# Optimization experiments

Hardware: AMD Instinct MI355X
Metric: run time of the kernel (lower is better)

The kernel has to match this reference:

```python
import jax, jax.numpy as jnp
import numpy as np

NC = 6            # CPAB tessellation cells (tess_size=6, zero_boundary=True)
DIM = NC - 1      # theta dimension = 5
SIG_LEN = 2048
CHANNELS = 3
BATCH = 256
FC_IN = 64 * 168  # flattened net_part1 output for signal_len=2048
NUM_SCALING = 0   # N in transform_data_ss
EPS_BN = 1e-5


def _cpab_basis():
    """QR null-space basis of the CPAB continuity + zero-boundary constraints.
    Params ordered [a_1,b_1,...,a_NC,b_NC]; v(x)=a_c x + b_c on cell c."""
    nc = NC
    L = np.zeros((nc + 1, 2 * nc))
    for k in range(1, nc):  # continuity at internal knots x_k = k/nc
        xk = k / nc
        L[k - 1, 2 * (k - 1)] = xk
        L[k - 1, 2 * (k - 1) + 1] = 1.0
        L[k - 1, 2 * k] = -xk
        L[k - 1, 2 * k + 1] = -1.0
    L[nc - 1, 1] = 1.0        # v(0) = 0  -> b_1 = 0
    L[nc, 2 * (nc - 1)] = 1.0  # v(1) = 0 -> a_nc + b_nc = 0
    L[nc, 2 * nc - 1] = 1.0
    Q, _ = np.linalg.qr(L.T, mode='complete')
    return np.ascontiguousarray(Q[:, nc + 1:]).astype(np.float32)  # (12, 5)


def _conv1d(x, w, b):
    y = jax.lax.conv_general_dilated(x, w, (1,), 'VALID',
                                     dimension_numbers=('NCH', 'OIH', 'NCH'))
    return y + b[None, :, None]


def _maxpool1d(x, k, s):
    return jax.lax.reduce_window(x, -jnp.inf, jax.lax.max, (1, 1, k), (1, 1, s), 'VALID')


def _bn(x, g, b, m, v):  # eval-mode BatchNorm1d
    return (x - m[None, :, None]) * (g / jnp.sqrt(v + EPS_BN))[None, :, None] + b[None, :, None]


def _integrate(x, A):
    """Exact CPAB 1D flow integration over t=1 with cell-crossing handling.
    x: (B, n) points in [0,1]; A: (B, NC, 2) per-cell (a, b). Monotone
    trajectories cross at most NC-1 boundaries -> fixed NC+1 iterations."""
    a_all, b_all = A[:, :, 0], A[:, :, 1]
    t = jnp.ones_like(x)
    for _ in range(NC + 1):
        c = jnp.clip(jnp.floor(x * NC).astype(jnp.int32), 0, NC - 1)
        a = jnp.take_along_axis(a_all, c, axis=1)
        b = jnp.take_along_axis(b_all, c, axis=1)
        v = a * x + b
        xb = jnp.where(v >= 0, (c + 1).astype(x.dtype) / NC, c.astype(x.dtype) / NC)
        big_a = jnp.abs(a) > 1e-8
        a_s = jnp.where(big_a, a, 1.0)
        z = x + b / a_s        # shifted coord: x(t) = z*exp(a t) - b/a
        zb = xb + b / a_s
        ratio = zb / jnp.where(jnp.abs(z) > 1e-12, z, 1e-12)
        t_exp = jnp.log(jnp.maximum(ratio, 1e-12)) / a_s
        v_s = jnp.where(jnp.abs(v) > 1e-12, v, 1.0)
        t_lin = (xb - x) / v_s
        thit = jnp.where(big_a, t_exp, t_lin)
        valid = (jnp.abs(v) > 1e-12) & (thit > 0) & (jnp.where(big_a, ratio, 1.0) > 0)
        thit = jnp.where(valid, thit, jnp.inf)
        tau = jnp.minimum(t, thit)
        x_new = jnp.where(big_a, z * jnp.exp(a * tau) - (z - x), x + b * tau)
        hit = thit <= t
        nudge = jnp.where(v >= 0, 1e-6, -1e-6)  # push into next cell
        x = jnp.clip(jnp.where(hit, xb + nudge, x_new), 0.0, 1.0)
        t = jnp.maximum(t - tau, 0.0)
    return x


def _interp1d(data, pos):
    """data: (B, L, C); pos: (B, n) in [0,1] -> (B, n, C) linear interpolation."""
    Lw = data.shape[1]
    p = jnp.clip(pos, 0.0, 1.0) * (Lw - 1)
    x0 = jnp.clip(jnp.floor(p).astype(jnp.int32), 0, Lw - 2)
    w = (p - x0.astype(p.dtype))[:, :, None]
    d0 = jnp.take_along_axis(data, x0[:, :, None], axis=1)
    d1 = jnp.take_along_axis(data, (x0 + 1)[:, :, None], axis=1)
    return d0 * (1.0 - w) + d1 * w


def _transform_data_ss(data, theta, basis, outsize, N):
    """CPAB scaling-and-squaring warp of data (B, L, C) by theta (B, DIM)."""
    Bsz = theta.shape[0]
    A = (theta @ basis.T).reshape(Bsz, NC, 2) / (2.0 ** N)
    grid = jnp.linspace(0.0, 1.0, outsize, dtype=data.dtype)
    grid_t = _integrate(jnp.broadcast_to(grid, (Bsz, outsize)), A)
    for _ in range(N):  # squaring: compose the warp with itself
        grid_t = _interp1d(grid_t[:, :, None], grid_t)[:, :, 0]
    return _interp1d(data, grid_t)


def reference(x, conv1_w, conv1_b, bn1_g, bn1_b, bn1_m, bn1_v,
              conv2_w, conv2_b, bn2_g, bn2_b, bn2_m, bn2_v,
              conv3_w, conv3_b, bn3_g, bn3_b, bn3_m, bn3_v,
              fc1_w, fc1_b, fc2_w, fc2_b, fc3_w, fc3_b, fc4_w, fc4_b, basis):
    # localization net (n_recurrence = 1, back_version = True)
    h = jax.nn.relu(_maxpool1d(_bn(_conv1d(x, conv1_w, conv1_b), bn1_g, bn1_b, bn1_m, bn1_v), 3, 2))
    h = jax.nn.relu(_maxpool1d(_bn(_conv1d(h, conv2_w, conv2_b), bn2_g, bn2_b, bn2_m, bn2_v), 3, 3))
    h = jax.nn.relu(_maxpool1d(_bn(_conv1d(h, conv3_w, conv3_b), bn3_g, bn3_b, bn3_m, bn3_v), 3, 2))
    xs = h.reshape(h.shape[0], -1)  # (B, 64*168)
    xs = jax.nn.relu(xs @ fc1_w.T + fc1_b)
    xs = jax.nn.relu(xs @ fc2_w.T + fc2_b)
    xs = jax.nn.relu(xs @ fc3_w.T + fc3_b)
    theta = jnp.tanh(xs @ fc4_w.T + fc4_b)  # (B, 5)
    data = jnp.transpose(x, (0, 2, 1))       # (B, L, C)
    warped = _transform_data_ss(data, theta, basis, SIG_LEN, NUM_SCALING)
    return jnp.transpose(warped, (0, 2, 1))  # (B, C, L)


def setup_inputs() -> dict:
    key = jax.random.key(0)
    ks = jax.random.split(key, 16)
    def nrm(k, shape, scale):
        return (jax.random.normal(k, shape) * scale).astype(jnp.float32)
    inp = {}
    inp['x'] = jax.random.normal(ks[0], (BATCH, CHANNELS, SIG_LEN), dtype=jnp.float32)
    inp['conv1_w'] = nrm(ks[1], (128, CHANNELS, 3), (CHANNELS * 3) ** -0.5)
    inp['conv1_b'] = nrm(ks[2], (128,), 0.01)
    inp['bn1_g'] = jnp.ones((128,), jnp.float32)
    inp['bn1_b'] = jnp.zeros((128,), jnp.float32)
    inp['bn1_m'] = nrm(ks[3], (128,), 0.1)
    inp['bn1_v'] = jnp.ones((128,), jnp.float32)
    inp['conv2_w'] = nrm(ks[4], (64, 128, 5), (128 * 5) ** -0.5)
    inp['conv2_b'] = nrm(ks[5], (64,), 0.01)
    inp['bn2_g'] = jnp.ones((64,), jnp.float32)
    inp['bn2_b'] = jnp.zeros((64,), jnp.float32)
    inp['bn2_m'] = nrm(ks[6], (64,), 0.1)
    inp['bn2_v'] = jnp.ones((64,), jnp.float32)
    inp['conv3_w'] = nrm(ks[7], (64, 64, 3), (64 * 3) ** -0.5)
    inp['conv3_b'] = nrm(ks[8], (64,), 0.01)
    inp['bn3_g'] = jnp.ones((64,), jnp.float32)
    inp['bn3_b'] = jnp.zeros((64,), jnp.float32)
    inp['bn3_m'] = nrm(ks[9], (64,), 0.1)
    inp['bn3_v'] = jnp.ones((64,), jnp.float32)
    inp['fc1_w'] = nrm(ks[10], (48, FC_IN), FC_IN ** -0.5)
    inp['fc1_b'] = jnp.zeros((48,), jnp.float32)
    inp['fc2_w'] = nrm(ks[11], (32, 48), 48 ** -0.5)
    inp['fc2_b'] = jnp.zeros((32,), jnp.float32)
    inp['fc3_w'] = nrm(ks[12], (16, 32), 32 ** -0.5)
    inp['fc3_b'] = jnp.zeros((16,), jnp.float32)
    # near-identity warp head (original zero-inits weight, identity bias)
    inp['fc4_w'] = nrm(ks[13], (DIM, 16), 0.01)
    inp['fc4_b'] = nrm(ks[14], (DIM,), 0.01)
    inp['basis'] = jnp.asarray(_cpab_basis())
    return inp
```

## Files before the change

kernel.cpp:

```cpp
#include <hip/hip_runtime.h>
#include <math.h>

#define BATCH   256
#define SIGLEN  2048
#define L1OUT   1022
#define L2OUT   339
#define L3OUT   168
#define FCIN    10752

#define TP2   21
#define NROW  68
#define H1S   136

#define TU3   28

#define KC1   12
#define KCL   (FCIN/KC1)

typedef float f32x4  __attribute__((ext_vector_type(4)));
typedef float f32x16 __attribute__((ext_vector_type(16)));
typedef short s16x8  __attribute__((ext_vector_type(8)));

__device__ __forceinline__ unsigned short f2bf(float f) {
    unsigned int u = __float_as_uint(f);
    return (unsigned short)((u + 0x7fffu + ((u >> 16) & 1u)) >> 16);
}
__device__ __forceinline__ float bf2f(unsigned short h) {
    return __uint_as_float(((unsigned int)h) << 16);
}

__launch_bounds__(256)
__global__ void prep_kernel(
    const float* __restrict__ conv1_b,
    const float* __restrict__ g1, const float* __restrict__ b1,
    const float* __restrict__ m1, const float* __restrict__ v1,
    const float* __restrict__ conv2_w, const float* __restrict__ conv2_b,
    const float* __restrict__ g2, const float* __restrict__ b2,
    const float* __restrict__ m2, const float* __restrict__ v2,
    const float* __restrict__ conv3_w, const float* __restrict__ conv3_b,
    const float* __restrict__ g3, const float* __restrict__ b3,
    const float* __restrict__ m3, const float* __restrict__ v3,
    const float* __restrict__ fc1_w,
    unsigned short* __restrict__ w2hi, unsigned short* __restrict__ w2lo,
    unsigned short* __restrict__ w3hi, unsigned short* __restrict__ w3lo,
    float* __restrict__ wp1,
    float* __restrict__ so1, float* __restrict__ so2, float* __restrict__ so3)
{
    int tid = blockIdx.x * 256 + threadIdx.x;
    int stride = gridDim.x * 256;
    for (int i = tid; i < 64*128*5; i += stride) {
        int co = i / 640; int rr = i - co*640; int ci = rr / 5; int k = rr - ci*5;
        float w = conv2_w[i];
        unsigned short hi = f2bf(w);
        unsigned short lo = f2bf(w - bf2f(hi));
        int seg = k*8 + (ci >> 4);
        int dst = ((seg*2 + (co >> 5))*32 + (co & 31))*16 + (ci & 15);
        w2hi[dst] = hi;
        w2lo[dst] = lo;
    }
    for (int i = tid; i < 64*64*3; i += stride) {
        int co = i / 192; int r = i - co*192; int ci = r / 3; int k = r - ci*3;
        float w = conv3_w[i];
        unsigned short hi = f2bf(w);
        unsigned short lo = f2bf(w - bf2f(hi));
        int dst = ((k*2 + (ci >> 5))*64 + co)*32 + (ci & 31);
        w3hi[dst] = hi;
        w3lo[dst] = lo;
    }
    for (int i = tid; i < 48*FCIN; i += stride) {
        int o = i / FCIN; int r = i - o*FCIN;
        int u = r >> 6, co = r & 63;
        wp1[i] = fc1_w[o*FCIN + co*L3OUT + u];
    }
    if (tid < 128) {
        float s = g1[tid] / sqrtf(v1[tid] + 1e-5f);
        so1[tid]       = s;
        so1[128 + tid] = (conv1_b[tid] - m1[tid]) * s + b1[tid];
    }
    if (tid < 64) {
        float s2 = g2[tid] / sqrtf(v2[tid] + 1e-5f);
        so2[tid]      = s2;
        so2[64 + tid] = (conv2_b[tid] - m2[tid]) * s2 + b2[tid];
        float s3 = g3[tid] / sqrtf(v3[tid] + 1e-5f);
        so3[tid]      = s3;
        so3[64 + tid] = (conv3_b[tid] - m3[tid]) * s3 + b3[tid];
    }
}

__launch_bounds__(256, 4)
__global__ void conv12_kernel(
    const float* __restrict__ x, const float* __restrict__ w1,
    const unsigned short* __restrict__ w2hi, const unsigned short* __restrict__ w2lo,
    const float* __restrict__ so1, const float* __restrict__ so2,
    unsigned int* __restrict__ h2p)
{
    __shared__ unsigned short h1hi[NROW * H1S];
    __shared__ unsigned short h1lo[NROW * H1S];

    int t  = threadIdx.x;
    int b  = blockIdx.x;
    int u0 = blockIdx.y * TP2;
    int q0 = 3 * u0;
    int wv = __builtin_amdgcn_readfirstlane(t >> 6);
    int l  = t & 63;

    float wr[2][9];
    float s1r[2], o1r[2];
    #pragma unroll
    for (int h = 0; h < 2; ++h) {
        int ch = l + 64*h;
        #pragma unroll
        for (int j = 0; j < 9; ++j) wr[h][j] = w1[ch*9 + j];
        s1r[h] = so1[ch]; o1r[h] = so1[128 + ch];
    }
    for (int s = 0; s < 17; ++s) {
        int r = 4*s + wv;
        int xbase = 2*(q0 + r);
        float xv[3][5];
        #pragma unroll
        for (int ci = 0; ci < 3; ++ci) {
            const float* xp = x + (b*3 + ci)*SIGLEN;
            #pragma unroll
            for (int d = 0; d < 5; ++d) {
                int xi = xbase + d; xi = xi < SIGLEN ? xi : SIGLEN - 1;
                xv[ci][d] = xp[xi];
            }
        }
        #pragma unroll
        for (int h = 0; h < 2; ++h) {
            float r0 = 0.f, r1 = 0.f, r2 = 0.f;
            #pragma unroll
            for (int ci = 0; ci < 3; ++ci) {
                float wA = wr[h][ci*3], wB = wr[h][ci*3+1], wC = wr[h][ci*3+2];
                r0 = fmaf(xv[ci][0], wA, fmaf(xv[ci][1], wB, fmaf(xv[ci][2], wC, r0)));
                r1 = fmaf(xv[ci][1], wA, fmaf(xv[ci][2], wB, fmaf(xv[ci][3], wC, r1)));
                r2 = fmaf(xv[ci][2], wA, fmaf(xv[ci][3], wB, fmaf(xv[ci][4], wC, r2)));
            }
            float mx = fmaxf(r0, fmaxf(r1, r2));
            float v  = fmaxf(fmaf(s1r[h], mx, o1r[h]), 0.f);
            unsigned short hi = f2bf(v);
            unsigned short lo = f2bf(v - bf2f(hi));
            h1hi[r*H1S + l + 64*h] = hi;
            h1lo[r*H1S + l + 64*h] = lo;
        }
    }
    __syncthreads();

    int chf = wv & 1;
    int kh  = wv >> 1;
    int r32 = l & 31;
    int oct = l >> 5;

    f32x16 acc0 = (f32x16)(0.f);
    f32x16 acc1 = (f32x16)(0.f);
    const unsigned short* whB = w2hi + (chf*32 + r32)*16 + oct*8;
    const unsigned short* wlB = w2lo + (chf*32 + r32)*16 + oct*8;

    #pragma unroll 4
    for (int ss = 0; ss < 20; ++ss) {
        int sg = kh*20 + ss;
        int ks = sg >> 3, cb = sg & 7;
        s16x8 wh = *(const s16x8*)(whB + sg*1024);
        s16x8 wl = *(const s16x8*)(wlB + sg*1024);
        int row0 = r32 + ks;
        int row1 = 32 + r32 + ks;
        s16x8 ah0 = *(const s16x8*)&h1hi[row0*H1S + cb*16 + oct*8];
        s16x8 al0 = *(const s16x8*)&h1lo[row0*H1S + cb*16 + oct*8];
        s16x8 ah1 = *(const s16x8*)&h1hi[row1*H1S + cb*16 + oct*8];
        s16x8 al1 = *(const s16x8*)&h1lo[row1*H1S + cb*16 + oct*8];
        acc0 = __builtin_amdgcn_mfma_f32_32x32x16_bf16(ah0, wh, acc0, 0, 0, 0);
        acc1 = __builtin_amdgcn_mfma_f32_32x32x16_bf16(ah1, wh, acc1, 0, 0, 0);
        acc0 = __builtin_amdgcn_mfma_f32_32x32x16_bf16(al0, wh, acc0, 0, 0, 0);
        acc1 = __builtin_amdgcn_mfma_f32_32x32x16_bf16(al1, wh, acc1, 0, 0, 0);
        acc0 = __builtin_amdgcn_mfma_f32_32x32x16_bf16(ah0, wl, acc0, 0, 0, 0);
        acc1 = __builtin_amdgcn_mfma_f32_32x32x16_bf16(ah1, wl, acc1, 0, 0, 0);
    }
    __syncthreads();

    float* c2 = (float*)h1hi;
    if (kh == 0) {
        #pragma unroll
        for (int rg = 0; rg < 16; ++rg) {
            int row = (rg & 3) + 8*(rg >> 2) + 4*oct;
            c2[row*65        + chf*32 + r32] = acc0[rg];
            c2[(32 + row)*65 + chf*32 + r32] = acc1[rg];
        }
    }
    __syncthreads();
    if (kh == 1) {
        #pragma unroll
        for (int rg = 0; rg < 16; ++rg) {
            int row = (rg & 3) + 8*(rg >> 2) + 4*oct;
            c2[row*65        + chf*32 + r32] += acc0[rg];
            c2[(32 + row)*65 + chf*32 + r32] += acc1[rg];
        }
    }
    __syncthreads();

    #pragma unroll
    for (int it = 0; it < 6; ++it) {
        int idx = t + it*256;
        if (idx < TP2*64) {
            int ul = idx >> 6, co = idx & 63;
            int u = u0 + ul;
            if (u < L2OUT) {
                float v0 = c2[(3*ul  )*65 + co];
                float v1 = c2[(3*ul+1)*65 + co];
                float v2 = c2[(3*ul+2)*65 + co];
                float mm = fmaxf(v0, fmaxf(v1, v2));
                float v  = fmaxf(fmaf(so2[co], mm, so2[64 + co]), 0.f);
                unsigned short hi = f2bf(v);
                unsigned short lo = f2bf(v - bf2f(hi));
                h2p[(b*L2OUT + u)*64 + co] = (unsigned int)hi | ((unsigned int)lo << 16);
            }
        }
    }
}

__launch_bounds__(256, 4)
__global__ void conv3_kernel(
    const unsigned int* __restrict__ h2p,
    const unsigned short* __restrict__ w3hi, const unsigned short* __restrict__ w3lo,
    const float* __restrict__ so3, float* __restrict__ xs)
{
    __shared__ unsigned short h3hi[66 * 72];
    __shared__ unsigned short h3lo[66 * 72];

    int t  = threadIdx.x;
    int b  = blockIdx.x;
    int u0 = blockIdx.y * TU3;
    int wv = __builtin_amdgcn_readfirstlane(t >> 6);
    int l  = t & 63;
    int m  = l & 15;
    int qd = l >> 4;

    for (int i = t; i < 66*64; i += 256) {
        int r = i >> 6, ci = i & 63;
        int g = 2*u0 + r; g = g > (L2OUT-1) ? (L2OUT-1) : g;
        unsigned int v = h2p[(b*L2OUT + g)*64 + ci];
        h3hi[r*72 + ci] = (unsigned short)(v & 0xffffu);
        h3lo[r*72 + ci] = (unsigned short)(v >> 16);
    }
    __syncthreads();

    s16x8 wh[6], wl[6];
    #pragma unroll
    for (int s = 0; s < 6; ++s) {
        wh[s] = *(const s16x8*)(w3hi + s*2048 + (wv*16 + m)*32 + qd*8);
        wl[s] = *(const s16x8*)(w3lo + s*2048 + (wv*16 + m)*32 + qd*8);
    }

    f32x4 acc[4] = {(f32x4)(0.f), (f32x4)(0.f), (f32x4)(0.f), (f32x4)(0.f)};
    #pragma unroll
    for (int pt = 0; pt < 4; ++pt) {
        #pragma unroll
        for (int s = 0; s < 6; ++s) {
            int row = pt*16 + m + (s >> 1);
            int off = (s & 1)*32 + qd*8;
            s16x8 ah = *(const s16x8*)&h3hi[row*72 + off];
            s16x8 al = *(const s16x8*)&h3lo[row*72 + off];
            acc[pt] = __builtin_amdgcn_mfma_f32_16x16x32_bf16(ah, wh[s], acc[pt], 0, 0, 0);
            acc[pt] = __builtin_amdgcn_mfma_f32_16x16x32_bf16(al, wh[s], acc[pt], 0, 0, 0);
            acc[pt] = __builtin_amdgcn_mfma_f32_16x16x32_bf16(ah, wl[s], acc[pt], 0, 0, 0);
        }
    }
    __syncthreads();

    float* c3 = (float*)h3hi;
    #pragma unroll
    for (int pt = 0; pt < 4; ++pt)
        #pragma unroll
        for (int rg = 0; rg < 4; ++rg)
            c3[(pt*16 + qd*4 + rg)*65 + wv*16 + m] = acc[pt][rg];
    __syncthreads();

    #pragma unroll
    for (int it = 0; it < 7; ++it) {
        int idx = t + it*256;
        if (idx < TU3*64) {
            int ul = idx >> 6, co = idx & 63;
            int p = 2*ul;
            float v0 = c3[(p  )*65 + co];
            float v1 = c3[(p+1)*65 + co];
            float v2 = c3[(p+2)*65 + co];
            float mm = fmaxf(v0, fmaxf(v1, v2));
            xs[b*FCIN + (u0 + ul)*64 + co] = fmaxf(fmaf(so3[co], mm, so3[64 + co]), 0.f);
        }
    }
}

__launch_bounds__(256)
__global__ void fc1_kernel(
    const float* __restrict__ xs, const float* __restrict__ w,
    float* __restrict__ part)
{
    int t = threadIdx.x, lane = t & 63, wid = t >> 6;
    int b0 = blockIdx.x * 4;
    int kc = blockIdx.y;
    int o0 = wid * 12;
    float acc[48];
    #pragma unroll
    for (int i = 0; i < 48; ++i) acc[i] = 0.f;

    int kbase = kc * KCL + lane;
    for (int ki = 0; ki < KCL/64; ++ki) {
        int k = kbase + ki * 64;
        float xv0 = xs[(b0 + 0) * FCIN + k];
        float xv1 = xs[(b0 + 1) * FCIN + k];
        float xv2 = xs[(b0 + 2) * FCIN + k];
        float xv3 = xs[(b0 + 3) * FCIN + k];
        #pragma unroll
        for (int j = 0; j < 12; ++j) {
            float ww = w[(o0 + j) * FCIN + k];
            acc[j]      += xv0 * ww;
            acc[12 + j] += xv1 * ww;
            acc[24 + j] += xv2 * ww;
            acc[36 + j] += xv3 * ww;
        }
    }
    #pragma unroll
    for (int i = 0; i < 48; ++i) {
        #pragma unroll
        for (int off = 32; off > 0; off >>= 1)
            acc[i] += __shfl_xor(acc[i], off, 64);
    }
    if (lane == 0) {
        #pragma unroll
        for (int bb = 0; bb < 4; ++bb)
            #pragma unroll
            for (int j = 0; j < 12; ++j)
                part[((b0 + bb) * 48 + o0 + j) * KC1 + kc] = acc[bb * 12 + j];
    }
}

__launch_bounds__(256)
__global__ void warp_kernel(
    const float* __restrict__ x, const float* __restrict__ part,
    const float* __restrict__ fc1_b,
    const float* __restrict__ fc2_w, const float* __restrict__ fc2_b,
    const float* __restrict__ fc3_w, const float* __restrict__ fc3_b,
    const float* __restrict__ fc4_w, const float* __restrict__ fc4_b,
    const float* __restrict__ basis,
    float* __restrict__ out)
{
    __shared__ float xsl[48];
    __shared__ float hl[32];
    __shared__ float gl[16];
    __shared__ float thl[5];
    __shared__ float Al[12];

    int b = blockIdx.x;
    int t = threadIdx.x;
    int i = blockIdx.y * 256 + t;

    if (t < 48) {
        const float4* p = (const float4*)&part[(b * 48 + t) * KC1];
        float4 pa = p[0], pb = p[1], pc = p[2];
        float sv = ((pa.x + pa.y) + (pa.z + pa.w))
                 + ((pb.x + pb.y) + (pb.z + pb.w))
                 + ((pc.x + pc.y) + (pc.z + pc.w));
        xsl[t] = fmaxf(sv + fc1_b[t], 0.f);
    }
    __syncthreads();
    if (t < 32) {
        float sv = fc2_b[t];
        #pragma unroll
        for (int k = 0; k < 48; ++k) sv = fmaf(fc2_w[t * 48 + k], xsl[k], sv);
        hl[t] = fmaxf(sv, 0.f);
    }
    __syncthreads();
    if (t < 16) {
        float sv = fc3_b[t];
        #pragma unroll
        for (int k = 0; k < 32; ++k) sv = fmaf(fc3_w[t * 32 + k], hl[k], sv);
        gl[t] = fmaxf(sv, 0.f);
    }
    __syncthreads();
    if (t < 5) {
        float sv = fc4_b[t];
        #pragma unroll
        for (int k = 0; k < 16; ++k) sv = fmaf(fc4_w[t * 16 + k], gl[k], sv);
        thl[t] = tanhf(sv);
    }
    __syncthreads();
    if (t < 12) {
        float sv = 0.f;
        #pragma unroll
        for (int d = 0; d < 5; ++d) sv = fmaf(basis[t * 5 + d], thl[d], sv);
        Al[t] = sv;
    }
    __syncthreads();

    float xp = (float)i / 2047.f;
    float tt = 1.f;
    for (int it = 0; it < 7; ++it) {
        int c = (int)floorf(xp * 6.f);
        c = min(max(c, 0), 5);
        float a  = Al[2 * c], bb = Al[2 * c + 1];
        float v  = a * xp + bb;
        float xb = (v >= 0.f) ? (float)(c + 1) / 6.f : (float)c / 6.f;
        bool  big_a = fabsf(a) > 1e-8f;
        float a_s = big_a ? a : 1.f;
        float z   = xp + bb / a_s;
        float zb  = xb + bb / a_s;
        float zden = (fabsf(z) > 1e-12f) ? z : 1e-12f;
        float ratio = zb / zden;
        float t_exp = logf(fmaxf(ratio, 1e-12f)) / a_s;
        float v_s   = (fabsf(v) > 1e-12f) ? v : 1.f;
        float t_lin = (xb - xp) / v_s;
        float thit  = big_a ? t_exp : t_lin;
        bool valid  = (fabsf(v) > 1e-12f) && (thit > 0.f) && ((big_a ? ratio : 1.f) > 0.f);
        if (!valid) thit = __builtin_inff();
        float tau   = fminf(tt, thit);
        float x_new = big_a ? (z * expf(a * tau) - (z - xp)) : (xp + bb * tau);
        bool hit    = (thit <= tt);
        float nudge = (v >= 0.f) ? 1e-6f : -1e-6f;
        xp = hit ? (xb + nudge) : x_new;
        xp = fminf(fmaxf(xp, 0.f), 1.f);
        tt = fmaxf(tt - tau, 0.f);
    }
    float p = fminf(fmaxf(xp, 0.f), 1.f) * 2047.f;
    int i0 = (int)floorf(p);
    i0 = min(max(i0, 0), 2046);
    float w = p - (float)i0;
    #pragma unroll
    for (int c = 0; c < 3; ++c) {
        const float* d = &x[(b * 3 + c) * SIGLEN];
        out[(b * 3 + c) * SIGLEN + i] = d[i0] * (1.f - w) + d[i0 + 1] * w;
    }
}

extern "C" void kernel_launch(void* const* d_in, const int* in_sizes, int n_in,
                              void* d_out, int out_size, void* d_ws, size_t ws_size,
                              hipStream_t stream) {
    (void)in_sizes; (void)n_in; (void)out_size; (void)ws_size;
    const float* x       = (const float*)d_in[0];
    const float* conv1_w = (const float*)d_in[1];
    const float* conv1_b = (const float*)d_in[2];
    const float* bn1_g   = (const float*)d_in[3];
    const float* bn1_b   = (const float*)d_in[4];
    const float* bn1_m   = (const float*)d_in[5];
    const float* bn1_v   = (const float*)d_in[6];
    const float* conv2_w = (const float*)d_in[7];
    const float* conv2_b = (const float*)d_in[8];
    const float* bn2_g   = (const float*)d_in[9];
    const float* bn2_b   = (const float*)d_in[10];
    const float* bn2_m   = (const float*)d_in[11];
    const float* bn2_v   = (const float*)d_in[12];
    const float* conv3_w = (const float*)d_in[13];
    const float* conv3_b = (const float*)d_in[14];
    const float* bn3_g   = (const float*)d_in[15];
    const float* bn3_b   = (const float*)d_in[16];
    const float* bn3_m   = (const float*)d_in[17];
    const float* bn3_v   = (const float*)d_in[18];
    const float* fc1_w   = (const float*)d_in[19];
    const float* fc1_b   = (const float*)d_in[20];
    const float* fc2_w   = (const float*)d_in[21];
    const float* fc2_b   = (const float*)d_in[22];
    const float* fc3_w   = (const float*)d_in[23];
    const float* fc3_b   = (const float*)d_in[24];
    const float* fc4_w   = (const float*)d_in[25];
    const float* fc4_b   = (const float*)d_in[26];
    const float* basis   = (const float*)d_in[27];

    unsigned short* w2hi = (unsigned short*)d_ws;
    unsigned short* w2lo = w2hi + 40960;
    unsigned short* w3hi = w2lo + 40960;
    unsigned short* w3lo = w3hi + 12288;
    float* ws   = (float*)d_ws;
    float* so1  = ws + 53248;
    float* so2  = so1 + 256;
    float* so3  = so2 + 128;
    float* wp1  = so3 + 128;
    unsigned int* h2p = (unsigned int*)(wp1 + 516096);
    float* xs   = wp1 + 516096 + 5554176;
    float* part = xs  + 2752512;

    prep_kernel<<<256, 256, 0, stream>>>(
        conv1_b, bn1_g, bn1_b, bn1_m, bn1_v,
        conv2_w, conv2_b, bn2_g, bn2_b, bn2_m, bn2_v,
        conv3_w, conv3_b, bn3_g, bn3_b, bn3_m, bn3_v,
        fc1_w, w2hi, w2lo, w3hi, w3lo, wp1, so1, so2, so3);

    dim3 g2(BATCH, (L2OUT + TP2 - 1) / TP2);
    conv12_kernel<<<g2, 256, 0, stream>>>(x, conv1_w, w2hi, w2lo, so1, so2, h2p);

    dim3 g3(BATCH, L3OUT / TU3);
    conv3_kernel<<<g3, 256, 0, stream>>>(h2p, w3hi, w3lo, so3, xs);

    dim3 gfc(BATCH / 4, KC1);
    fc1_kernel<<<gfc, 256, 0, stream>>>(xs, wp1, part);

    dim3 g5(BATCH, SIGLEN / 256);
    warp_kernel<<<g5, 256, 0, stream>>>(x, part, fc1_b, fc2_w, fc2_b,
                                        fc3_w, fc3_b, fc4_w, fc4_b, basis,
                                        (float*)d_out);
}
```

Measured before the change: 262.2 us.

## Drop fc1 weight permutation, write conv3 output in native layout, merge warp blocks

conv3 now writes its activations in the channel-major order that fc1_w already uses, so the prep kernel no longer permutes the 2 MB fc1 weight matrix each call, and fc1 reads fc1_w directly. The conv12 kernel stores both K-half partial sums to separate shared buffers and adds them in the pooling step, which replaces a two-phase accumulate and removes one barrier. The warp kernel runs one block per batch row that loops over 8 chunks with per-cell coefficients held in registers, cutting redundant recomputation of the FC head. The trade-offs are strided global writes in conv3 and lower parallelism in the warp kernel.

```diff
diff --git a/kernel.cpp b/kernel.cpp
--- a/kernel.cpp
+++ b/kernel.cpp
@@ -11,6 +11,7 @@
 #define TP2   21
 #define NROW  68
 #define H1S   136
+#define H1SZ  (NROW*H1S)
 
 #define TU3   28
 
@@ -40,10 +41,8 @@
     const float* __restrict__ conv3_w, const float* __restrict__ conv3_b,
     const float* __restrict__ g3, const float* __restrict__ b3,
     const float* __restrict__ m3, const float* __restrict__ v3,
-    const float* __restrict__ fc1_w,
     unsigned short* __restrict__ w2hi, unsigned short* __restrict__ w2lo,
     unsigned short* __restrict__ w3hi, unsigned short* __restrict__ w3lo,
-    float* __restrict__ wp1,
     float* __restrict__ so1, float* __restrict__ so2, float* __restrict__ so3)
 {
     int tid = blockIdx.x * 256 + threadIdx.x;
@@ -67,11 +66,6 @@
         w3hi[dst] = hi;
         w3lo[dst] = lo;
     }
-    for (int i = tid; i < 48*FCIN; i += stride) {
-        int o = i / FCIN; int r = i - o*FCIN;
-        int u = r >> 6, co = r & 63;
-        wp1[i] = fc1_w[o*FCIN + co*L3OUT + u];
-    }
     if (tid < 128) {
         float s = g1[tid] / sqrtf(v1[tid] + 1e-5f);
         so1[tid]       = s;
@@ -94,8 +88,7 @@
     const float* __restrict__ so1, const float* __restrict__ so2,
     unsigned int* __restrict__ h2p)
 {
-    __shared__ unsigned short h1hi[NROW * H1S];
-    __shared__ unsigned short h1lo[NROW * H1S];
+    __shared__ unsigned short h1s[2 * H1SZ];
 
     int t  = threadIdx.x;
     int b  = blockIdx.x;
@@ -140,8 +133,8 @@
             float v  = fmaxf(fmaf(s1r[h], mx, o1r[h]), 0.f);
             unsigned short hi = f2bf(v);
             unsigned short lo = f2bf(v - bf2f(hi));
-            h1hi[r*H1S + l + 64*h] = hi;
-            h1lo[r*H1S + l + 64*h] = lo;
+            h1s[r*H1S + l + 64*h]        = hi;
+            h1s[H1SZ + r*H1S + l + 64*h] = lo;
         }
     }
     __syncthreads();
@@ -164,10 +157,10 @@
         s16x8 wl = *(const s16x8*)(wlB + sg*1024);
         int row0 = r32 + ks;
         int row1 = 32 + r32 + ks;
-        s16x8 ah0 = *(const s16x8*)&h1hi[row0*H1S + cb*16 + oct*8];
-        s16x8 al0 = *(const s16x8*)&h1lo[row0*H1S + cb*16 + oct*8];
-        s16x8 ah1 = *(const s16x8*)&h1hi[row1*H1S + cb*16 + oct*8];
-        s16x8 al1 = *(const s16x8*)&h1lo[row1*H1S + cb*16 + oct*8];
+        s16x8 ah0 = *(const s16x8*)&h1s[row0*H1S + cb*16 + oct*8];
+        s16x8 al0 = *(const s16x8*)&h1s[H1SZ + row0*H1S + cb*16 + oct*8];
+        s16x8 ah1 = *(const s16x8*)&h1s[row1*H1S + cb*16 + oct*8];
+        s16x8 al1 = *(const s16x8*)&h1s[H1SZ + row1*H1S + cb*16 + oct*8];
         acc0 = __builtin_amdgcn_mfma_f32_32x32x16_bf16(ah0, wh, acc0, 0, 0, 0);
         acc1 = __builtin_amdgcn_mfma_f32_32x32x16_bf16(ah1, wh, acc1, 0, 0, 0);
         acc0 = __builtin_amdgcn_mfma_f32_32x32x16_bf16(al0, wh, acc0, 0, 0, 0);
@@ -177,23 +170,12 @@
     }
     __syncthreads();
 
-    float* c2 = (float*)h1hi;
-    if (kh == 0) {
-        #pragma unroll
-        for (int rg = 0; rg < 16; ++rg) {
-            int row = (rg & 3) + 8*(rg >> 2) + 4*oct;
-            c2[row*65        + chf*32 + r32] = acc0[rg];
-            c2[(32 + row)*65 + chf*32 + r32] = acc1[rg];
-        }
-    }
-    __syncthreads();
-    if (kh == 1) {
-        #pragma unroll
-        for (int rg = 0; rg < 16; ++rg) {
-            int row = (rg & 3) + 8*(rg >> 2) + 4*oct;
-            c2[row*65        + chf*32 + r32] += acc0[rg];
-            c2[(32 + row)*65 + chf*32 + r32] += acc1[rg];
-        }
+    float* c2 = (float*)h1s;
+    #pragma unroll
+    for (int rg = 0; rg < 16; ++rg) {
+        int row = (rg & 3) + 8*(rg >> 2) + 4*oct;
+        c2[kh*4160 + row*65        + chf*32 + r32] = acc0[rg];
+        c2[kh*4160 + (32 + row)*65 + chf*32 + r32] = acc1[rg];
     }
     __syncthreads();
 
@@ -204,9 +186,9 @@
             int ul = idx >> 6, co = idx & 63;
             int u = u0 + ul;
             if (u < L2OUT) {
-                float v0 = c2[(3*ul  )*65 + co];
-                float v1 = c2[(3*ul+1)*65 + co];
-                float v2 = c2[(3*ul+2)*65 + co];
+                float v0 = c2[(3*ul  )*65 + co] + c2[4160 + (3*ul  )*65 + co];
+                float v1 = c2[(3*ul+1)*65 + co] + c2[4160 + (3*ul+1)*65 + co];
+                float v2 = c2[(3*ul+2)*65 + co] + c2[4160 + (3*ul+2)*65 + co];
                 float mm = fmaxf(v0, fmaxf(v1, v2));
                 float v  = fmaxf(fmaf(so2[co], mm, so2[64 + co]), 0.f);
                 unsigned short hi = f2bf(v);
@@ -278,13 +260,13 @@
     for (int it = 0; it < 7; ++it) {
         int idx = t + it*256;
         if (idx < TU3*64) {
-            int ul = idx >> 6, co = idx & 63;
+            int co = idx / TU3, ul = idx - co*TU3;
             int p = 2*ul;
             float v0 = c3[(p  )*65 + co];
             float v1 = c3[(p+1)*65 + co];
             float v2 = c3[(p+2)*65 + co];
             float mm = fmaxf(v0, fmaxf(v1, v2));
-            xs[b*FCIN + (u0 + ul)*64 + co] = fmaxf(fmaf(so3[co], mm, so3[64 + co]), 0.f);
+            xs[b*FCIN + co*L3OUT + (u0 + ul)] = fmaxf(fmaf(so3[co], mm, so3[64 + co]), 0.f);
         }
     }
 }
@@ -351,7 +333,6 @@
 
     int b = blockIdx.x;
     int t = threadIdx.x;
-    int i = blockIdx.y * 256 + t;
 
     if (t < 48) {
         const float4* p = (const float4*)&part[(b * 48 + t) * KC1];
@@ -391,42 +372,49 @@
     }
     __syncthreads();
 
-    float xp = (float)i / 2047.f;
-    float tt = 1.f;
-    for (int it = 0; it < 7; ++it) {
-        int c = (int)floorf(xp * 6.f);
-        c = min(max(c, 0), 5);
-        float a  = Al[2 * c], bb = Al[2 * c + 1];
-        float v  = a * xp + bb;
-        float xb = (v >= 0.f) ? (float)(c + 1) / 6.f : (float)c / 6.f;
-        bool  big_a = fabsf(a) > 1e-8f;
-        float a_s = big_a ? a : 1.f;
-        float z   = xp + bb / a_s;
-        float zb  = xb + bb / a_s;
-        float zden = (fabsf(z) > 1e-12f) ? z : 1e-12f;
-        float ratio = zb / zden;
-        float t_exp = logf(fmaxf(ratio, 1e-12f)) / a_s;
-        float v_s   = (fabsf(v) > 1e-12f) ? v : 1.f;
-        float t_lin = (xb - xp) / v_s;
-        float thit  = big_a ? t_exp : t_lin;
-        bool valid  = (fabsf(v) > 1e-12f) && (thit > 0.f) && ((big_a ? ratio : 1.f) > 0.f);
-        if (!valid) thit = __builtin_inff();
-        float tau   = fminf(tt, thit);
-        float x_new = big_a ? (z * expf(a * tau) - (z - xp)) : (xp + bb * tau);
-        bool hit    = (thit <= tt);
-        float nudge = (v >= 0.f) ? 1e-6f : -1e-6f;
-        xp = hit ? (xb + nudge) : x_new;
-        xp = fminf(fmaxf(xp, 0.f), 1.f);
-        tt = fmaxf(tt - tau, 0.f);
-    }
-    float p = fminf(fmaxf(xp, 0.f), 1.f) * 2047.f;
-    int i0 = (int)floorf(p);
-    i0 = min(max(i0, 0), 2046);
-    float w = p - (float)i0;
-    #pragma unroll
-    for (int c = 0; c < 3; ++c) {
-        const float* d = &x[(b * 3 + c) * SIGLEN];
-        out[(b * 3 + c) * SIGLEN + i] = d[i0] * (1.f - w) + d[i0 + 1] * w;
+    float a_r[6], b_r[6];
+    #pragma unroll
+    for (int c = 0; c < 6; ++c) { a_r[c] = Al[2*c]; b_r[c] = Al[2*c+1]; }
+
+    for (int ch = 0; ch < 8; ++ch) {
+        int i = ch * 256 + t;
+        float xp = (float)i / 2047.f;
+        float tt = 1.f;
+        for (int it = 0; it < 7; ++it) {
+            int c = (int)floorf(xp * 6.f);
+            c = min(max(c, 0), 5);
+            float a  = a_r[c], bb = b_r[c];
+            float v  = a * xp + bb;
+            float xb = (v >= 0.f) ? (float)(c + 1) / 6.f : (float)c / 6.f;
+            bool  big_a = fabsf(a) > 1e-8f;
+            float a_s = big_a ? a : 1.f;
+            float z   = xp + bb / a_s;
+            float zb  = xb + bb / a_s;
+            float zden = (fabsf(z) > 1e-12f) ? z : 1e-12f;
+            float ratio = zb / zden;
+            float t_exp = logf(fmaxf(ratio, 1e-12f)) / a_s;
+            float v_s   = (fabsf(v) > 1e-12f) ? v : 1.f;
+            float t_lin = (xb - xp) / v_s;
+            float thit  = big_a ? t_exp : t_lin;
+            bool valid  = (fabsf(v) > 1e-12f) && (thit > 0.f) && ((big_a ? ratio : 1.f) > 0.f);
+            if (!valid) thit = __builtin_inff();
+            float tau   = fminf(tt, thit);
+            float x_new = big_a ? (z * expf(a * tau) - (z - xp)) : (xp + bb * tau);
+            bool hit    = (thit <= tt);
+            float nudge = (v >= 0.f) ? 1e-6f : -1e-6f;
+            xp = hit ? (xb + nudge) : x_new;
+            xp = fminf(fmaxf(xp, 0.f), 1.f);
+            tt = fmaxf(tt - tau, 0.f);
+        }
+        float p = fminf(fmaxf(xp, 0.f), 1.f) * 2047.f;
+        int i0 = (int)floorf(p);
+        i0 = min(max(i0, 0), 2046);
+        float w = p - (float)i0;
+        #pragma unroll
+        for (int c = 0; c < 3; ++c) {
+            const float* d = &x[(b * 3 + c) * SIGLEN];
+            out[(b * 3 + c) * SIGLEN + i] = d[i0] * (1.f - w) + d[i0 + 1] * w;
+        }
     }
 }
 
@@ -471,16 +459,15 @@
     float* so1  = ws + 53248;
     float* so2  = so1 + 256;
     float* so3  = so2 + 128;
-    float* wp1  = so3 + 128;
-    unsigned int* h2p = (unsigned int*)(wp1 + 516096);
-    float* xs   = wp1 + 516096 + 5554176;
-    float* part = xs  + 2752512;
-
-    prep_kernel<<<256, 256, 0, stream>>>(
+    unsigned int* h2p = (unsigned int*)(so3 + 128);
+    float* xs   = (float*)(h2p + 5554176);
+    float* part = xs + 2752512;
+
+    prep_kernel<<<64, 256, 0, stream>>>(
         conv1_b, bn1_g, bn1_b, bn1_m, bn1_v,
         conv2_w, conv2_b, bn2_g, bn2_b, bn2_m, bn2_v,
         conv3_w, conv3_b, bn3_g, bn3_b, bn3_m, bn3_v,
-        fc1_w, w2hi, w2lo, w3hi, w3lo, wp1, so1, so2, so3);
+        w2hi, w2lo, w3hi, w3lo, so1, so2, so3);
 
     dim3 g2(BATCH, (L2OUT + TP2 - 1) / TP2);
     conv12_kernel<<<g2, 256, 0, stream>>>(x, conv1_w, w2hi, w2lo, so1, so2, h2p);
@@ -489,10 +476,9 @@
     conv3_kernel<<<g3, 256, 0, stream>>>(h2p, w3hi, w3lo, so3, xs);
 
     dim3 gfc(BATCH / 4, KC1);
-    fc1_kernel<<<gfc, 256, 0, stream>>>(xs, wp1, part);
-
-    dim3 g5(BATCH, SIGLEN / 256);
-    warp_kernel<<<g5, 256, 0, stream>>>(x, part, fc1_b, fc2_w, fc2_b,
-                                        fc3_w, fc3_b, fc4_w, fc4_b, basis,
-                                        (float*)d_out);
-}
+    fc1_kernel<<<gfc, 256, 0, stream>>>(xs, fc1_w, part);
+
+    warp_kernel<<<BATCH, 256, 0, stream>>>(x, part, fc1_b, fc2_w, fc2_b,
+                                           fc3_w, fc3_b, fc4_w, fc4_b, basis,
+                                           (float*)d_out);
+}
```

After: 268.4 us. +2.4%, slower.
